# Kernel optimization log

Measured on AMD Instinct MI355X. Metric: run time of the kernel, lower is better.

## Reference

```python
import jax, jax.numpy as jnp
import numpy as np
import math

L, B = 1024, 256
SEQ_DIM, KMER_DIM, HID = 16, 256, 64
N_LAYERS = 2
IN_DIM = SEQ_DIM + KMER_DIM + 21  # 293


def _normalize(v, eps=1e-12):
    return v / jnp.maximum(jnp.linalg.norm(v, axis=-1, keepdims=True), eps)


def _nerf_rot(a, b, c):
    # rotation matrix with columns [bc, n x bc, n] from last three backbone points
    bc = _normalize(c - b)
    n = _normalize(jnp.cross(b - a, bc))
    return jnp.stack([bc, jnp.cross(n, bc), n], axis=-1)  # (..., 3, 3)


def pnerf(c_tilde, nfrag):
    # c_tilde: (3L, B, 3) SRF coordinates; parallelized natural extension of reference frame
    Ltot, batch = c_tilde.shape[0], c_tilde.shape[1]
    k = Ltot // nfrag
    # contiguous fragments of length k, folded into the batch dim: (k, nfrag*B, 3)
    x = c_tilde.reshape(nfrag, k, batch, 3).transpose(1, 0, 2, 3).reshape(k, nfrag * batch, 3)
    init = jnp.array([[-math.sqrt(0.5), math.sqrt(1.5), 0.0],
                      [-math.sqrt(2.0), 0.0, 0.0],
                      [0.0, 0.0, 0.0]], dtype=c_tilde.dtype)
    F = nfrag * batch
    carry0 = (jnp.broadcast_to(init[0], (F, 3)),
              jnp.broadcast_to(init[1], (F, 3)),
              jnp.broadcast_to(init[2], (F, 3)))

    def extend(carry, ct):
        a, b, c = carry
        R = _nerf_rot(a, b, c)                      # (F, 3, 3)
        d = c + jnp.einsum('fij,fj->fi', R, ct)     # (F, 3)
        return (b, c, d), d

    _, frag = jax.lax.scan(extend, carry0, x)        # (k, F, 3)
    frag = frag.reshape(k, nfrag, batch, 3).transpose(1, 0, 2, 3)  # (nfrag, k, B, 3)

    # assemble fragments sequentially; init frame is identity/origin so frag 0 passes through
    carryA = (jnp.broadcast_to(init[0], (batch, 3)),
              jnp.broadcast_to(init[1], (batch, 3)),
              jnp.broadcast_to(init[2], (batch, 3)))

    def assemble(carry, fr):
        a, b, c = carry
        R = _nerf_rot(a, b, c)                      # (B, 3, 3)
        y = c + jnp.einsum('bij,kbj->kbi', R, fr)   # (k, B, 3)
        return (y[-3], y[-2], y[-1]), y

    _, ys = jax.lax.scan(assemble, carryA, frag)     # (nfrag, k, B, 3)
    return ys.reshape(nfrag * k, batch, 3)


def setup_inputs() -> dict:
    key = jax.random.key(0)
    ks = jax.random.split(key, 12)
    s = 0.05
    return {
        'seq': jax.random.randint(ks[0], (L, B), 0, 20, dtype=jnp.int64),
        'kmer': jax.random.randint(ks[1], (L, B), 0, 22 ** 3, dtype=jnp.int64),
        'pssm': jax.random.uniform(ks[2], (L, B, 21), dtype=jnp.float32),
        'length': jax.random.randint(ks[3], (L,), 1, L, dtype=jnp.int64),
        'seq_embed': jax.random.normal(ks[4], (20, SEQ_DIM), dtype=jnp.float32) * s,
        'kmer_embed': jax.random.normal(ks[5], (22 ** 3, KMER_DIM), dtype=jnp.float32) * s,
        'W0': jax.random.normal(ks[6], (IN_DIM, HID), dtype=jnp.float32) * s,
        'b0': jnp.zeros((HID,), dtype=jnp.float32),
        'We': jax.random.normal(ks[7], (HID, HID), dtype=jnp.float32) * s,
        'be': jnp.zeros((HID,), dtype=jnp.float32),
        'W1': jax.random.normal(ks[8], (HID, 9), dtype=jnp.float32) * s,
        'b1': jnp.zeros((9,), dtype=jnp.float32),
    }


def reference(seq, kmer, pssm, length, seq_embed, kmer_embed, W0, b0, We, be, W1, b1):
    s = seq_embed[seq]                                   # (L, B, 16)
    km = kmer_embed[kmer]                                # (L, B, 256)
    h = jnp.concatenate([s, km, pssm], axis=2)           # (L, B, 293)
    h = h @ W0 + b0                                      # (L, B, 64)
    # torch list-multiplication shares the SAME Linear across the n_layers blocks
    for _ in range(N_LAYERS):
        h = jax.nn.relu(h @ We + be)                     # dropout is identity at eval
    srf = h @ W1 + b1                                    # (L, B, 9)
    Ld, Bd = srf.shape[0], srf.shape[1]
    srf = srf.reshape(Ld, Bd, 3, 3).transpose(0, 2, 1, 3).reshape(3 * Ld, Bd, 3)
    return pnerf(srf, int(math.sqrt(Ld)))
```

## Files before the change

### kernel.cpp

```cpp
#include <hip/hip_runtime.h>
#include <math.h>

#define HPAD 72
#define PPAD 40

typedef short bf16x8 __attribute__((ext_vector_type(8)));
typedef float f32x4  __attribute__((ext_vector_type(4)));

__device__ __forceinline__ unsigned short f2bf(float x) {
    unsigned int u = __float_as_uint(x);
    return (unsigned short)((u + 0x7FFFu + ((u >> 16) & 1u)) >> 16);
}
__device__ __forceinline__ float bf2f(unsigned short h) {
    return __uint_as_float(((unsigned int)h) << 16);
}
__device__ __forceinline__ void split2(float x, unsigned short& h, unsigned short& l) {
    h = f2bf(x);
    l = f2bf(x - bf2f(h));
}

__device__ __forceinline__ float inv_norm3(float x, float y, float z) {
    float d = fmaf(x, x, fmaf(y, y, z * z));
    return rsqrtf(fmaxf(d, 1e-24f));
}
__device__ __forceinline__ float3 f3sub(float3 a, float3 b) {
    return make_float3(a.x - b.x, a.y - b.y, a.z - b.z);
}
__device__ __forceinline__ float3 f3cross(float3 a, float3 b) {
    return make_float3(a.y * b.z - a.z * b.y,
                       a.z * b.x - a.x * b.z,
                       a.x * b.y - a.y * b.x);
}
__device__ __forceinline__ void nerf_frame(const float3& A, const float3& Bv,
                                           const float3& C, float3& bc,
                                           float3& n, float3& m3) {
    float3 w  = f3sub(C, Bv);
    float3 v  = f3sub(Bv, A);
    float3 cr = f3cross(v, w);
    float iw = inv_norm3(w.x, w.y, w.z);
    float ic = inv_norm3(cr.x, cr.y, cr.z);
    bc = make_float3(w.x * iw, w.y * iw, w.z * iw);
    n  = make_float3(cr.x * ic, cr.y * ic, cr.z * ic);
    m3 = f3cross(n, bc);
}
__device__ __forceinline__ float3 nerf_place(const float3& C, const float3& bc,
                                             const float3& m3, const float3& n,
                                             float tx, float ty, float tz) {
    return make_float3(
        fmaf(m3.x, ty, fmaf(bc.x, tx, fmaf(n.x, tz, C.x))),
        fmaf(m3.y, ty, fmaf(bc.y, tx, fmaf(n.y, tz, C.y))),
        fmaf(m3.z, ty, fmaf(bc.z, tx, fmaf(n.z, tz, C.z))));
}

__global__ __launch_bounds__(64) void seq_table_kernel(
    const float* __restrict__ se, const float* __restrict__ W0,
    const float* __restrict__ b0, float* __restrict__ seqT) {
    int j = threadIdx.x;
    int r = blockIdx.x;
    float acc = b0[j];
    #pragma unroll
    for (int k = 0; k < 16; ++k)
        acc = fmaf(se[r * 16 + k], W0[k * 64 + j], acc);
    float cs = 0.f;
    #pragma unroll
    for (int c = 0; c < 21; ++c) cs += W0[(272 + c) * 64 + j];
    seqT[r * 64 + j] = acc + 0.5f * cs;
}

__global__ __launch_bounds__(256) void kmer_table_kernel(
    const float* __restrict__ emb, const float* __restrict__ W0,
    float* __restrict__ kt) {
    int j  = threadIdx.x & 63;
    int wv = threadIdx.x >> 6;
    int r0 = blockIdx.x * 44 + wv * 11;
    float acc[11] = {0.f,0.f,0.f,0.f,0.f,0.f,0.f,0.f,0.f,0.f,0.f};
    #pragma unroll 8
    for (int k = 0; k < 256; ++k) {
        float w = W0[(16 + k) * 64 + j];
        #pragma unroll
        for (int r = 0; r < 11; ++r)
            acc[r] = fmaf(emb[(r0 + r) * 256 + k], w, acc[r]);
    }
    #pragma unroll
    for (int r = 0; r < 11; ++r)
        kt[(r0 + r) * 64 + j] = acc[r];
}

__global__ __launch_bounds__(256, 3) void mlp_kernel(
    const int* __restrict__ seq, const int* __restrict__ kmer,
    const float* __restrict__ pssm,
    const float* __restrict__ seqT, const float* __restrict__ kmerT,
    const float* __restrict__ W0, const float* __restrict__ We,
    const float* __restrict__ be, const float* __restrict__ W1,
    const float* __restrict__ b1, float* __restrict__ srf_t) {

    __shared__ __align__(16) unsigned short Hah[64][HPAD];
    __shared__ __align__(16) unsigned short Hal[64][HPAD];
    __shared__ __align__(16) unsigned short ovl[2][64][HPAD];
    __shared__ int sidx[64];
    __shared__ int kidx[64];

    unsigned short (*Ph)[PPAD] = (unsigned short(*)[PPAD])(&ovl[0][0][0]);
    unsigned short (*Pl)[PPAD] = (unsigned short(*)[PPAD])(&ovl[0][0][0] + 2560);
    unsigned short (*Hbh)[HPAD] = ovl[0];
    unsigned short (*Hbl)[HPAD] = ovl[1];

    const int tid  = threadIdx.x;
    const int lane = tid & 63;
    const int wv   = __builtin_amdgcn_readfirstlane(tid >> 6);
    const int q    = lane >> 4;
    const int c16  = lane & 15;
    const int m0   = blockIdx.x * 64;
    const int n    = wv * 16 + c16;

    if (tid < 64) {
        sidx[tid] = seq[m0 + tid];
        kidx[tid] = kmer[m0 + tid];
    }
    for (int i = tid; i < 64 * 21; i += 256) {
        float v = pssm[m0 * 21 + i] - 0.5f;
        unsigned short h, l; split2(v, h, l);
        Ph[i / 21][i % 21] = h;
        Pl[i / 21][i % 21] = l;
    }
    for (int i = tid; i < 64 * 11; i += 256) {
        Ph[i / 11][21 + (i % 11)] = 0;
        Pl[i / 11][21 + (i % 11)] = 0;
    }

    bf16x8 WeH[2], WeL[2], W1H[2], W1L[2], W0H, W0L;
    #pragma unroll
    for (int kk = 0; kk < 2; ++kk)
        #pragma unroll
        for (int j = 0; j < 8; ++j) {
            float w = We[(kk * 32 + q * 8 + j) * 64 + n];
            unsigned short h, l; split2(w, h, l);
            WeH[kk][j] = (short)h; WeL[kk][j] = (short)l;
        }
    #pragma unroll
    for (int j = 0; j < 8; ++j) {
        int k = q * 8 + j;
        float w = (k < 21) ? W0[(272 + k) * 64 + n] : 0.f;
        unsigned short h, l; split2(w, h, l);
        W0H[j] = (short)h; W0L[j] = (short)l;
    }
    #pragma unroll
    for (int kk = 0; kk < 2; ++kk)
        #pragma unroll
        for (int j = 0; j < 8; ++j) {
            int k = kk * 32 + q * 8 + j;
            float w = (c16 < 9) ? W1[k * 9 + c16] : 0.f;
            unsigned short h, l; split2(w, h, l);
            W1H[kk][j] = (short)h; W1L[kk][j] = (short)l;
        }
    const float be_n = be[n];
    const float b1h  = (c16 < 9) ? b1[c16] : 0.f;
    __syncthreads();

    f32x4 acc[4];
    #pragma unroll
    for (int t = 0; t < 4; ++t) {
        #pragma unroll
        for (int r = 0; r < 4; ++r) {
            int m = t * 16 + q * 4 + r;
            acc[t][r] = seqT[sidx[m] * 64 + n] + kmerT[kidx[m] * 64 + n];
        }
    }
    #pragma unroll
    for (int t = 0; t < 4; ++t) {
        bf16x8 ah = *(const bf16x8*)&Ph[t * 16 + c16][q * 8];
        bf16x8 al = *(const bf16x8*)&Pl[t * 16 + c16][q * 8];
        acc[t] = __builtin_amdgcn_mfma_f32_16x16x32_bf16(ah, W0H, acc[t], 0, 0, 0);
        acc[t] = __builtin_amdgcn_mfma_f32_16x16x32_bf16(al, W0H, acc[t], 0, 0, 0);
        acc[t] = __builtin_amdgcn_mfma_f32_16x16x32_bf16(ah, W0L, acc[t], 0, 0, 0);
    }
    #pragma unroll
    for (int t = 0; t < 4; ++t)
        #pragma unroll
        for (int r = 0; r < 4; ++r) {
            unsigned short h, l; split2(acc[t][r], h, l);
            Hah[t * 16 + q * 4 + r][n] = h;
            Hal[t * 16 + q * 4 + r][n] = l;
        }
    __syncthreads();

    {
        f32x4 a1[4];
        #pragma unroll
        for (int t = 0; t < 4; ++t) {
            a1[t] = (f32x4){be_n, be_n, be_n, be_n};
            #pragma unroll
            for (int kk = 0; kk < 2; ++kk) {
                bf16x8 ah = *(const bf16x8*)&Hah[t * 16 + c16][kk * 32 + q * 8];
                bf16x8 al = *(const bf16x8*)&Hal[t * 16 + c16][kk * 32 + q * 8];
                a1[t] = __builtin_amdgcn_mfma_f32_16x16x32_bf16(ah, WeH[kk], a1[t], 0, 0, 0);
                a1[t] = __builtin_amdgcn_mfma_f32_16x16x32_bf16(al, WeH[kk], a1[t], 0, 0, 0);
                a1[t] = __builtin_amdgcn_mfma_f32_16x16x32_bf16(ah, WeL[kk], a1[t], 0, 0, 0);
            }
        }
        #pragma unroll
        for (int t = 0; t < 4; ++t)
            #pragma unroll
            for (int r = 0; r < 4; ++r) {
                unsigned short h, l; split2(fmaxf(a1[t][r], 0.f), h, l);
                Hbh[t * 16 + q * 4 + r][n] = h;
                Hbl[t * 16 + q * 4 + r][n] = l;
            }
        __syncthreads();
    }
    {
        f32x4 a2[4];
        #pragma unroll
        for (int t = 0; t < 4; ++t) {
            a2[t] = (f32x4){be_n, be_n, be_n, be_n};
            #pragma unroll
            for (int kk = 0; kk < 2; ++kk) {
                bf16x8 ah = *(const bf16x8*)&Hbh[t * 16 + c16][kk * 32 + q * 8];
                bf16x8 al = *(const bf16x8*)&Hbl[t * 16 + c16][kk * 32 + q * 8];
                a2[t] = __builtin_amdgcn_mfma_f32_16x16x32_bf16(ah, WeH[kk], a2[t], 0, 0, 0);
                a2[t] = __builtin_amdgcn_mfma_f32_16x16x32_bf16(al, WeH[kk], a2[t], 0, 0, 0);
                a2[t] = __builtin_amdgcn_mfma_f32_16x16x32_bf16(ah, WeL[kk], a2[t], 0, 0, 0);
            }
        }
        #pragma unroll
        for (int t = 0; t < 4; ++t)
            #pragma unroll
            for (int r = 0; r < 4; ++r) {
                unsigned short h, l; split2(fmaxf(a2[t][r], 0.f), h, l);
                Hah[t * 16 + q * 4 + r][n] = h;
                Hal[t * 16 + q * 4 + r][n] = l;
            }
        __syncthreads();
    }

    {
        f32x4 ah4 = (f32x4){b1h, b1h, b1h, b1h};
        #pragma unroll
        for (int kk = 0; kk < 2; ++kk) {
            bf16x8 ah = *(const bf16x8*)&Hah[wv * 16 + c16][kk * 32 + q * 8];
            bf16x8 al = *(const bf16x8*)&Hal[wv * 16 + c16][kk * 32 + q * 8];
            ah4 = __builtin_amdgcn_mfma_f32_16x16x32_bf16(ah, W1H[kk], ah4, 0, 0, 0);
            ah4 = __builtin_amdgcn_mfma_f32_16x16x32_bf16(al, W1H[kk], ah4, 0, 0, 0);
            ah4 = __builtin_amdgcn_mfma_f32_16x16x32_bf16(ah, W1L[kk], ah4, 0, 0, 0);
        }
        if (c16 < 9) {
            #pragma unroll
            for (int r = 0; r < 4; ++r) {
                int pos = m0 + wv * 16 + q * 4 + r;
                int l = pos >> 8, b = pos & 255;
                srf_t[(l * 9 + c16) * 256 + b] = ah4[r];
            }
        }
    }
}

__global__ __launch_bounds__(64) void extend_kernel(
    const float* __restrict__ srf_t, float* __restrict__ fragbuf) {
    int frag = blockIdx.x >> 2;
    int bb   = ((blockIdx.x & 3) << 6) + threadIdx.x;

    float3 A  = make_float3(-0.70710678118654752f, 1.22474487139158905f, 0.f);
    float3 Bv = make_float3(-1.41421356237309505f, 0.f, 0.f);
    float3 C  = make_float3(0.f, 0.f, 0.f);

    float ct[9];
    #pragma unroll
    for (int m = 0; m < 9; ++m)
        ct[m] = srf_t[((frag * 32) * 9 + m) * 256 + bb];

    for (int ll = 0; ll < 32; ++ll) {
        float nct[9];
        if (ll < 31) {
            #pragma unroll
            for (int m = 0; m < 9; ++m)
                nct[m] = srf_t[((frag * 32 + ll + 1) * 9 + m) * 256 + bb];
        } else {
            #pragma unroll
            for (int m = 0; m < 9; ++m) nct[m] = 0.f;
        }
        #pragma unroll
        for (int s3 = 0; s3 < 3; ++s3) {
            float3 bc, nn, m3;
            nerf_frame(A, Bv, C, bc, nn, m3);
            float3 d = nerf_place(C, bc, m3, nn,
                                  ct[3 * s3 + 0], ct[3 * s3 + 1], ct[3 * s3 + 2]);
            int row = frag * 96 + ll * 3 + s3;
            fragbuf[(row * 3 + 0) * 256 + bb] = d.x;
            fragbuf[(row * 3 + 1) * 256 + bb] = d.y;
            fragbuf[(row * 3 + 2) * 256 + bb] = d.z;
            A = Bv; Bv = C; C = d;
        }
        #pragma unroll
        for (int m = 0; m < 9; ++m) ct[m] = nct[m];
    }
}

__global__ __launch_bounds__(256) void carry_kernel(
    const float* __restrict__ fragbuf, float* __restrict__ frames) {
    int bb = threadIdx.x;
    float3 A  = make_float3(-0.70710678118654752f, 1.22474487139158905f, 0.f);
    float3 Bv = make_float3(-1.41421356237309505f, 0.f, 0.f);
    float3 C  = make_float3(0.f, 0.f, 0.f);

    float fr[9];
    #pragma unroll
    for (int t = 0; t < 3; ++t)
        #pragma unroll
        for (int c = 0; c < 3; ++c)
            fr[t * 3 + c] = fragbuf[((93 + t) * 3 + c) * 256 + bb];

    for (int frag = 0; frag < 32; ++frag) {
        float nfr[9];
        if (frag < 31) {
            #pragma unroll
            for (int t = 0; t < 3; ++t)
                #pragma unroll
                for (int c = 0; c < 3; ++c)
                    nfr[t * 3 + c] =
                        fragbuf[(((frag + 1) * 96 + 93 + t) * 3 + c) * 256 + bb];
        } else {
            #pragma unroll
            for (int m = 0; m < 9; ++m) nfr[m] = 0.f;
        }
        float3 bc, nn, m3;
        nerf_frame(A, Bv, C, bc, nn, m3);

        frames[(frag * 12 + 0)  * 256 + bb] = bc.x;
        frames[(frag * 12 + 1)  * 256 + bb] = bc.y;
        frames[(frag * 12 + 2)  * 256 + bb] = bc.z;
        frames[(frag * 12 + 3)  * 256 + bb] = m3.x;
        frames[(frag * 12 + 4)  * 256 + bb] = m3.y;
        frames[(frag * 12 + 5)  * 256 + bb] = m3.z;
        frames[(frag * 12 + 6)  * 256 + bb] = nn.x;
        frames[(frag * 12 + 7)  * 256 + bb] = nn.y;
        frames[(frag * 12 + 8)  * 256 + bb] = nn.z;
        frames[(frag * 12 + 9)  * 256 + bb] = C.x;
        frames[(frag * 12 + 10) * 256 + bb] = C.y;
        frames[(frag * 12 + 11) * 256 + bb] = C.z;

        float3 y[3];
        #pragma unroll
        for (int t = 0; t < 3; ++t)
            y[t] = nerf_place(C, bc, m3, nn, fr[t * 3], fr[t * 3 + 1], fr[t * 3 + 2]);
        A = y[0]; Bv = y[1]; C = y[2];
        #pragma unroll
        for (int m = 0; m < 9; ++m) fr[m] = nfr[m];
    }
}

__global__ __launch_bounds__(256) void apply_kernel(
    const float* __restrict__ fragbuf, const float* __restrict__ frames,
    float* __restrict__ out) {
    int bb   = threadIdx.x;
    int row  = blockIdx.x;
    int frag = row / 96;

    float fx = fragbuf[(row * 3 + 0) * 256 + bb];
    float fy = fragbuf[(row * 3 + 1) * 256 + bb];
    float fz = fragbuf[(row * 3 + 2) * 256 + bb];

    float bcx = frames[(frag * 12 + 0)  * 256 + bb];
    float bcy = frames[(frag * 12 + 1)  * 256 + bb];
    float bcz = frames[(frag * 12 + 2)  * 256 + bb];
    float mx  = frames[(frag * 12 + 3)  * 256 + bb];
    float my  = frames[(frag * 12 + 4)  * 256 + bb];
    float mz  = frames[(frag * 12 + 5)  * 256 + bb];
    float nx  = frames[(frag * 12 + 6)  * 256 + bb];
    float ny  = frames[(frag * 12 + 7)  * 256 + bb];
    float nz  = frames[(frag * 12 + 8)  * 256 + bb];
    float cx  = frames[(frag * 12 + 9)  * 256 + bb];
    float cy  = frames[(frag * 12 + 10) * 256 + bb];
    float cz  = frames[(frag * 12 + 11) * 256 + bb];

    out[(row * 256 + bb) * 3 + 0] = cx + bcx * fx + mx * fy + nx * fz;
    out[(row * 256 + bb) * 3 + 1] = cy + bcy * fx + my * fy + ny * fz;
    out[(row * 256 + bb) * 3 + 2] = cz + bcz * fx + mz * fy + nz * fz;
}

extern "C" void kernel_launch(void* const* d_in, const int* in_sizes, int n_in,
                              void* d_out, int out_size, void* d_ws, size_t ws_size,
                              hipStream_t stream) {
    const int*   seq        = (const int*)d_in[0];
    const int*   kmer       = (const int*)d_in[1];
    const float* pssm       = (const float*)d_in[2];
    const float* seq_embed  = (const float*)d_in[4];
    const float* kmer_embed = (const float*)d_in[5];
    const float* W0         = (const float*)d_in[6];
    const float* b0         = (const float*)d_in[7];
    const float* We         = (const float*)d_in[8];
    const float* be         = (const float*)d_in[9];
    const float* W1         = (const float*)d_in[10];
    const float* b1         = (const float*)d_in[11];

    float* ws      = (float*)d_ws;
    float* kmerT   = ws;
    float* seqT    = kmerT + 681472;
    float* srf_t   = seqT + 1280;
    float* fragbuf = srf_t + 2359296;
    float* frames  = fragbuf + 2359296;
    float* out     = (float*)d_out;

    hipLaunchKernelGGL(seq_table_kernel, dim3(20), dim3(64), 0, stream,
                       seq_embed, W0, b0, seqT);
    hipLaunchKernelGGL(kmer_table_kernel, dim3(242), dim3(256), 0, stream,
                       kmer_embed, W0, kmerT);
    hipLaunchKernelGGL(mlp_kernel, dim3(4096), dim3(256), 0, stream,
                       seq, kmer, pssm, seqT, kmerT, W0, We, be, W1, b1, srf_t);
    hipLaunchKernelGGL(extend_kernel, dim3(128), dim3(64), 0, stream,
                       srf_t, fragbuf);
    hipLaunchKernelGGL(carry_kernel, dim3(1), dim3(256), 0, stream,
                       fragbuf, frames);
    hipLaunchKernelGGL(apply_kernel, dim3(3072), dim3(256), 0, stream,
                       fragbuf, frames, out);
}
```

Measured before the change: 218.1 us.

## Precompute split bf16 weights, rebalance kmer table, vectorize frames, coalesce output

A new prep kernel computes the transposed hi/lo bf16 splits of We, W0 (pssm part) and W1 once, so each MLP block loads them as vector reads instead of redoing the splits. The hi-part split is replaced by a cheaper truncation, the kmer table kernel uses smaller per-wave row chunks over more blocks, frames are stored as float4 per batch element, and apply stages results in shared memory for coalesced output stores. The weight buffers live in fragbuf scratch space that extend_kernel later overwrites, which is safe given the launch order.

```diff
diff --git a/kernel.cpp b/kernel.cpp
--- a/kernel.cpp
+++ b/kernel.cpp
@@ -17,6 +17,12 @@
 __device__ __forceinline__ void split2(float x, unsigned short& h, unsigned short& l) {
     h = f2bf(x);
     l = f2bf(x - bf2f(h));
+}
+__device__ __forceinline__ void split2t(float x, unsigned short& h, unsigned short& l) {
+    unsigned int u = __float_as_uint(x);
+    h = (unsigned short)(u >> 16);
+    float r = x - __uint_as_float(u & 0xFFFF0000u);
+    l = f2bf(r);
 }
 
 __device__ __forceinline__ float inv_norm3(float x, float y, float z) {
@@ -52,19 +58,50 @@
         fmaf(m3.z, ty, fmaf(bc.z, tx, fmaf(n.z, tz, C.z))));
 }
 
-__global__ __launch_bounds__(64) void seq_table_kernel(
+__global__ __launch_bounds__(256) void prep_kernel(
     const float* __restrict__ se, const float* __restrict__ W0,
-    const float* __restrict__ b0, float* __restrict__ seqT) {
-    int j = threadIdx.x;
-    int r = blockIdx.x;
-    float acc = b0[j];
-    #pragma unroll
-    for (int k = 0; k < 16; ++k)
-        acc = fmaf(se[r * 16 + k], W0[k * 64 + j], acc);
-    float cs = 0.f;
-    #pragma unroll
-    for (int c = 0; c < 21; ++c) cs += W0[(272 + c) * 64 + j];
-    seqT[r * 64 + j] = acc + 0.5f * cs;
+    const float* __restrict__ b0, const float* __restrict__ We,
+    const float* __restrict__ W1, float* __restrict__ seqT,
+    unsigned short* __restrict__ WeTH, unsigned short* __restrict__ WeTL,
+    unsigned short* __restrict__ W0pTH, unsigned short* __restrict__ W0pTL,
+    unsigned short* __restrict__ W1TH, unsigned short* __restrict__ W1TL) {
+    int tid = threadIdx.x;
+    if (blockIdx.x < 5) {
+        int e = blockIdx.x * 256 + tid;
+        int r = e >> 6, j = e & 63;
+        float acc = b0[j];
+        #pragma unroll
+        for (int k = 0; k < 16; ++k)
+            acc = fmaf(se[r * 16 + k], W0[k * 64 + j], acc);
+        float cs = 0.f;
+        #pragma unroll
+        for (int c = 0; c < 21; ++c) cs += W0[(272 + c) * 64 + j];
+        seqT[r * 64 + j] = acc + 0.5f * cs;
+    } else {
+        #pragma unroll
+        for (int i = 0; i < 16; ++i) {
+            int e = i * 256 + tid;
+            int k = e >> 6, n = e & 63;
+            unsigned short h, l; split2(We[k * 64 + n], h, l);
+            WeTH[n * 64 + k] = h; WeTL[n * 64 + k] = l;
+        }
+        #pragma unroll
+        for (int i = 0; i < 8; ++i) {
+            int e = i * 256 + tid;
+            int k = e >> 6, n = e & 63;
+            float w = (k < 21) ? W0[(272 + k) * 64 + n] : 0.f;
+            unsigned short h, l; split2(w, h, l);
+            W0pTH[n * 32 + k] = h; W0pTL[n * 32 + k] = l;
+        }
+        #pragma unroll
+        for (int i = 0; i < 4; ++i) {
+            int e = i * 256 + tid;
+            int k = e >> 4, c = e & 15;
+            float w = (c < 9) ? W1[k * 9 + c] : 0.f;
+            unsigned short h, l; split2(w, h, l);
+            W1TH[c * 64 + k] = h; W1TL[c * 64 + k] = l;
+        }
+    }
 }
 
 __global__ __launch_bounds__(256) void kmer_table_kernel(
@@ -72,17 +109,18 @@
     float* __restrict__ kt) {
     int j  = threadIdx.x & 63;
     int wv = threadIdx.x >> 6;
-    int r0 = blockIdx.x * 44 + wv * 11;
-    float acc[11] = {0.f,0.f,0.f,0.f,0.f,0.f,0.f,0.f,0.f,0.f,0.f};
+    int r0 = blockIdx.x * 16 + wv * 4;
+    if (r0 >= 10648) return;
+    float acc[4] = {0.f, 0.f, 0.f, 0.f};
     #pragma unroll 8
     for (int k = 0; k < 256; ++k) {
         float w = W0[(16 + k) * 64 + j];
         #pragma unroll
-        for (int r = 0; r < 11; ++r)
+        for (int r = 0; r < 4; ++r)
             acc[r] = fmaf(emb[(r0 + r) * 256 + k], w, acc[r]);
     }
     #pragma unroll
-    for (int r = 0; r < 11; ++r)
+    for (int r = 0; r < 4; ++r)
         kt[(r0 + r) * 64 + j] = acc[r];
 }
 
@@ -90,9 +128,11 @@
     const int* __restrict__ seq, const int* __restrict__ kmer,
     const float* __restrict__ pssm,
     const float* __restrict__ seqT, const float* __restrict__ kmerT,
-    const float* __restrict__ W0, const float* __restrict__ We,
-    const float* __restrict__ be, const float* __restrict__ W1,
-    const float* __restrict__ b1, float* __restrict__ srf_t) {
+    const unsigned short* __restrict__ WeTH, const unsigned short* __restrict__ WeTL,
+    const unsigned short* __restrict__ W0pTH, const unsigned short* __restrict__ W0pTL,
+    const unsigned short* __restrict__ W1TH, const unsigned short* __restrict__ W1TL,
+    const float* __restrict__ be, const float* __restrict__ b1,
+    float* __restrict__ srf_t) {
 
     __shared__ __align__(16) unsigned short Hah[64][HPAD];
     __shared__ __align__(16) unsigned short Hal[64][HPAD];
@@ -119,7 +159,7 @@
     }
     for (int i = tid; i < 64 * 21; i += 256) {
         float v = pssm[m0 * 21 + i] - 0.5f;
-        unsigned short h, l; split2(v, h, l);
+        unsigned short h, l; split2t(v, h, l);
         Ph[i / 21][i % 21] = h;
         Pl[i / 21][i % 21] = l;
     }
@@ -130,29 +170,14 @@
 
     bf16x8 WeH[2], WeL[2], W1H[2], W1L[2], W0H, W0L;
     #pragma unroll
-    for (int kk = 0; kk < 2; ++kk)
-        #pragma unroll
-        for (int j = 0; j < 8; ++j) {
-            float w = We[(kk * 32 + q * 8 + j) * 64 + n];
-            unsigned short h, l; split2(w, h, l);
-            WeH[kk][j] = (short)h; WeL[kk][j] = (short)l;
-        }
-    #pragma unroll
-    for (int j = 0; j < 8; ++j) {
-        int k = q * 8 + j;
-        float w = (k < 21) ? W0[(272 + k) * 64 + n] : 0.f;
-        unsigned short h, l; split2(w, h, l);
-        W0H[j] = (short)h; W0L[j] = (short)l;
-    }
-    #pragma unroll
-    for (int kk = 0; kk < 2; ++kk)
-        #pragma unroll
-        for (int j = 0; j < 8; ++j) {
-            int k = kk * 32 + q * 8 + j;
-            float w = (c16 < 9) ? W1[k * 9 + c16] : 0.f;
-            unsigned short h, l; split2(w, h, l);
-            W1H[kk][j] = (short)h; W1L[kk][j] = (short)l;
-        }
+    for (int kk = 0; kk < 2; ++kk) {
+        WeH[kk] = *(const bf16x8*)(WeTH + n * 64 + kk * 32 + q * 8);
+        WeL[kk] = *(const bf16x8*)(WeTL + n * 64 + kk * 32 + q * 8);
+        W1H[kk] = *(const bf16x8*)(W1TH + c16 * 64 + kk * 32 + q * 8);
+        W1L[kk] = *(const bf16x8*)(W1TL + c16 * 64 + kk * 32 + q * 8);
+    }
+    W0H = *(const bf16x8*)(W0pTH + n * 32 + q * 8);
+    W0L = *(const bf16x8*)(W0pTL + n * 32 + q * 8);
     const float be_n = be[n];
     const float b1h  = (c16 < 9) ? b1[c16] : 0.f;
     __syncthreads();
@@ -178,7 +203,7 @@
     for (int t = 0; t < 4; ++t)
         #pragma unroll
         for (int r = 0; r < 4; ++r) {
-            unsigned short h, l; split2(acc[t][r], h, l);
+            unsigned short h, l; split2t(acc[t][r], h, l);
             Hah[t * 16 + q * 4 + r][n] = h;
             Hal[t * 16 + q * 4 + r][n] = l;
         }
@@ -202,7 +227,7 @@
         for (int t = 0; t < 4; ++t)
             #pragma unroll
             for (int r = 0; r < 4; ++r) {
-                unsigned short h, l; split2(fmaxf(a1[t][r], 0.f), h, l);
+                unsigned short h, l; split2t(fmaxf(a1[t][r], 0.f), h, l);
                 Hbh[t * 16 + q * 4 + r][n] = h;
                 Hbl[t * 16 + q * 4 + r][n] = l;
             }
@@ -226,7 +251,7 @@
         for (int t = 0; t < 4; ++t)
             #pragma unroll
             for (int r = 0; r < 4; ++r) {
-                unsigned short h, l; split2(fmaxf(a2[t][r], 0.f), h, l);
+                unsigned short h, l; split2t(fmaxf(a2[t][r], 0.f), h, l);
                 Hah[t * 16 + q * 4 + r][n] = h;
                 Hal[t * 16 + q * 4 + r][n] = l;
             }
@@ -296,7 +321,7 @@
 }
 
 __global__ __launch_bounds__(256) void carry_kernel(
-    const float* __restrict__ fragbuf, float* __restrict__ frames) {
+    const float* __restrict__ fragbuf, float4* __restrict__ frames) {
     int bb = threadIdx.x;
     float3 A  = make_float3(-0.70710678118654752f, 1.22474487139158905f, 0.f);
     float3 Bv = make_float3(-1.41421356237309505f, 0.f, 0.f);
@@ -325,18 +350,10 @@
         float3 bc, nn, m3;
         nerf_frame(A, Bv, C, bc, nn, m3);
 
-        frames[(frag * 12 + 0)  * 256 + bb] = bc.x;
-        frames[(frag * 12 + 1)  * 256 + bb] = bc.y;
-        frames[(frag * 12 + 2)  * 256 + bb] = bc.z;
-        frames[(frag * 12 + 3)  * 256 + bb] = m3.x;
-        frames[(frag * 12 + 4)  * 256 + bb] = m3.y;
-        frames[(frag * 12 + 5)  * 256 + bb] = m3.z;
-        frames[(frag * 12 + 6)  * 256 + bb] = nn.x;
-        frames[(frag * 12 + 7)  * 256 + bb] = nn.y;
-        frames[(frag * 12 + 8)  * 256 + bb] = nn.z;
-        frames[(frag * 12 + 9)  * 256 + bb] = C.x;
-        frames[(frag * 12 + 10) * 256 + bb] = C.y;
-        frames[(frag * 12 + 11) * 256 + bb] = C.z;
+        int fb = (frag * 256 + bb) * 3;
+        frames[fb + 0] = make_float4(bc.x, bc.y, bc.z, m3.x);
+        frames[fb + 1] = make_float4(m3.y, m3.z, nn.x, nn.y);
+        frames[fb + 2] = make_float4(nn.z, C.x, C.y, C.z);
 
         float3 y[3];
         #pragma unroll
@@ -349,8 +366,9 @@
 }
 
 __global__ __launch_bounds__(256) void apply_kernel(
-    const float* __restrict__ fragbuf, const float* __restrict__ frames,
+    const float* __restrict__ fragbuf, const float4* __restrict__ frames,
     float* __restrict__ out) {
+    __shared__ float sm[768];
     int bb   = threadIdx.x;
     int row  = blockIdx.x;
     int frag = row / 96;
@@ -359,22 +377,20 @@
     float fy = fragbuf[(row * 3 + 1) * 256 + bb];
     float fz = fragbuf[(row * 3 + 2) * 256 + bb];
 
-    float bcx = frames[(frag * 12 + 0)  * 256 + bb];
-    float bcy = frames[(frag * 12 + 1)  * 256 + bb];
-    float bcz = frames[(frag * 12 + 2)  * 256 + bb];
-    float mx  = frames[(frag * 12 + 3)  * 256 + bb];
-    float my  = frames[(frag * 12 + 4)  * 256 + bb];
-    float mz  = frames[(frag * 12 + 5)  * 256 + bb];
-    float nx  = frames[(frag * 12 + 6)  * 256 + bb];
-    float ny  = frames[(frag * 12 + 7)  * 256 + bb];
-    float nz  = frames[(frag * 12 + 8)  * 256 + bb];
-    float cx  = frames[(frag * 12 + 9)  * 256 + bb];
-    float cy  = frames[(frag * 12 + 10) * 256 + bb];
-    float cz  = frames[(frag * 12 + 11) * 256 + bb];
-
-    out[(row * 256 + bb) * 3 + 0] = cx + bcx * fx + mx * fy + nx * fz;
-    out[(row * 256 + bb) * 3 + 1] = cy + bcy * fx + my * fy + ny * fz;
-    out[(row * 256 + bb) * 3 + 2] = cz + bcz * fx + mz * fy + nz * fz;
+    int fb = (frag * 256 + bb) * 3;
+    float4 f0 = frames[fb + 0];
+    float4 f1 = frames[fb + 1];
+    float4 f2 = frames[fb + 2];
+
+    sm[bb * 3 + 0] = f2.y + f0.x * fx + f0.w * fy + f1.z * fz;
+    sm[bb * 3 + 1] = f2.z + f0.y * fx + f1.x * fy + f1.w * fz;
+    sm[bb * 3 + 2] = f2.w + f0.z * fx + f1.y * fy + f2.x * fz;
+    __syncthreads();
+
+    int base = row * 768;
+    out[base + bb]       = sm[bb];
+    out[base + 256 + bb] = sm[256 + bb];
+    out[base + 512 + bb] = sm[512 + bb];
 }
 
 extern "C" void kernel_launch(void* const* d_in, const int* in_sizes, int n_in,
@@ -400,16 +416,26 @@
     float* frames  = fragbuf + 2359296;
     float* out     = (float*)d_out;
 
-    hipLaunchKernelGGL(seq_table_kernel, dim3(20), dim3(64), 0, stream,
-                       seq_embed, W0, b0, seqT);
-    hipLaunchKernelGGL(kmer_table_kernel, dim3(242), dim3(256), 0, stream,
+    unsigned short* WeTH  = (unsigned short*)fragbuf;
+    unsigned short* WeTL  = WeTH + 4096;
+    unsigned short* W0pTH = WeTL + 4096;
+    unsigned short* W0pTL = W0pTH + 2048;
+    unsigned short* W1TH  = W0pTL + 2048;
+    unsigned short* W1TL  = W1TH + 1024;
+
+    hipLaunchKernelGGL(prep_kernel, dim3(6), dim3(256), 0, stream,
+                       seq_embed, W0, b0, We, W1, seqT,
+                       WeTH, WeTL, W0pTH, W0pTL, W1TH, W1TL);
+    hipLaunchKernelGGL(kmer_table_kernel, dim3(666), dim3(256), 0, stream,
                        kmer_embed, W0, kmerT);
     hipLaunchKernelGGL(mlp_kernel, dim3(4096), dim3(256), 0, stream,
-                       seq, kmer, pssm, seqT, kmerT, W0, We, be, W1, b1, srf_t);
+                       seq, kmer, pssm, seqT, kmerT,
+                       WeTH, WeTL, W0pTH, W0pTL, W1TH, W1TL,
+                       be, b1, srf_t);
     hipLaunchKernelGGL(extend_kernel, dim3(128), dim3(64), 0, stream,
                        srf_t, fragbuf);
     hipLaunchKernelGGL(carry_kernel, dim3(1), dim3(256), 0, stream,
-                       fragbuf, frames);
+                       fragbuf, (float4*)frames);
     hipLaunchKernelGGL(apply_kernel, dim3(3072), dim3(256), 0, stream,
-                       fragbuf, frames, out);
-}
+                       fragbuf, (float4*)frames, out);
+}
```

Measured after the change: 222.1 us. Within noise of the previous version (+1.8%).
